# Kernel tuning notes

Measured on AMD Instinct MI355X. Metric: run time of the kernel, lower is better.

## Reference

```python
import jax, jax.numpy as jnp
import numpy as np

B, N, M = 8, 1024, 1024
D_MODEL, D_HEAD, M_BITS = 1024, 128, 32
SCALE = 1.0 / np.sqrt(M_BITS)


def setup_inputs() -> dict:
    key = jax.random.key(0)
    ks = jax.random.split(key, 11)
    w_std = 1.0 / np.sqrt(D_MODEL)  # ~ nn.Linear init scale
    f32 = jnp.float32
    return {
        "Q": jax.random.normal(ks[0], (B, N, D_MODEL), dtype=f32),
        "K": jax.random.normal(ks[1], (B, M, D_MODEL), dtype=f32),
        "V": jax.random.normal(ks[2], (B, M, D_MODEL), dtype=f32),
        "Wq_boolean": jax.random.normal(ks[3], (D_MODEL, M_BITS), dtype=f32) * w_std,
        "Wk_boolean": jax.random.normal(ks[4], (D_MODEL, M_BITS), dtype=f32) * w_std,
        "Wq_tropical": jax.random.normal(ks[5], (D_MODEL, M_BITS), dtype=f32) * w_std,
        "Wk_tropical": jax.random.normal(ks[6], (D_MODEL, M_BITS), dtype=f32) * w_std,
        "Wq_real": jax.random.normal(ks[7], (D_MODEL, M_BITS), dtype=f32) * w_std,
        "Wk_real": jax.random.normal(ks[8], (D_MODEL, M_BITS), dtype=f32) * w_std,
        "Wv": jax.random.normal(ks[9], (D_MODEL, D_HEAD), dtype=f32) * w_std,
        "fusion_weights": jnp.ones((3,), dtype=f32),
        "mask": jnp.ones((B, N, M), dtype=jnp.int32),
    }


def _tropical_sim(Qe, Ke):
    # max-plus (tropical) witness similarity: sim[b,n,m] = max_d (Qe[b,n,d] + Ke[b,m,d])
    # loop over the small fixed bit dim (M_BITS=32) to avoid a [B,N,M,M_BITS] tensor
    acc = Qe[:, :, 0][:, :, None] + Ke[:, :, 0][:, None, :]
    for b in range(1, M_BITS):
        acc = jnp.maximum(acc, Qe[:, :, b][:, :, None] + Ke[:, :, b][:, None, :])
    return acc  # [B,N,M]


def reference(Q, K, V, Wq_boolean, Wk_boolean, Wq_tropical, Wk_tropical,
              Wq_real, Wk_real, Wv, fusion_weights, mask):
    # --- boolean monoid: hard-binarized codes, bit-match count ---
    Qb = (Q @ Wq_boolean > 0).astype(Q.dtype)   # [B,N,m]
    Kb = (K @ Wk_boolean > 0).astype(K.dtype)   # [B,M,m]
    sim_bool = (jnp.einsum('bnd,bmd->bnm', Qb, Kb)
                + jnp.einsum('bnd,bmd->bnm', 1.0 - Qb, 1.0 - Kb))
    # --- tropical monoid: max-plus over continuous codes ---
    sim_trop = _tropical_sim(Q @ Wq_tropical, K @ Wk_tropical)
    # --- real monoid: inner product of continuous codes ---
    sim_real = jnp.einsum('bnd,bmd->bnm', Q @ Wq_real, K @ Wk_real)
    # --- learned fusion + scaled softmax attention ---
    w = jax.nn.softmax(fusion_weights)
    scores = (w[0] * sim_bool + w[1] * sim_trop + w[2] * sim_real) * SCALE
    scores = jnp.where(mask == 0, -jnp.inf, scores)
    attn = jax.nn.softmax(scores, axis=-1)     # [B,N,M]  (dropout: eval mode, identity)
    out = jnp.einsum('bnm,bmh->bnh', attn, V @ Wv)  # [B,N,d_head]
    return out, attn
```

## Files before the change

kernel.cpp:

```cpp
#include <hip/hip_runtime.h>
#include <stdint.h>
#include <math.h>


#define SCALE_F 0.17677669529663687f

typedef float4 f4;

__device__ __forceinline__ float f4c(const f4 v, int i) {
    return i == 0 ? v.x : (i == 1 ? v.y : (i == 2 ? v.z : v.w));
}


__global__ __launch_bounds__(256)
void proj_qk_kernel(const float* __restrict__ Q, const float* __restrict__ K,
                    const float* __restrict__ Wqb, const float* __restrict__ Wkb,
                    const float* __restrict__ Wqt, const float* __restrict__ Wkt,
                    const float* __restrict__ Wqr, const float* __restrict__ Wkr,
                    float* __restrict__ Pq, float* __restrict__ Pk) {
    const int t = threadIdx.x;
    const int bx = blockIdx.x;
    const int by = blockIdx.y;
    const int side = blockIdx.z;
    const float* __restrict__ X  = side ? K   : Q;
    const float* __restrict__ Wb = side ? Wkb : Wqb;
    const float* __restrict__ Wt = side ? Wkt : Wqt;
    const float* __restrict__ Wr = side ? Wkr : Wqr;
    float* __restrict__ P = side ? Pk : Pq;

    __shared__ float Xs[128][68];
    __shared__ float Ws[64][96];

    const int r0 = bx * 128;
    const int rt = t >> 3;
    const int cg = t & 7;

    float acc[4][12];
    #pragma unroll
    for (int i = 0; i < 4; ++i)
        #pragma unroll
        for (int j = 0; j < 12; ++j) acc[i][j] = 0.f;

    for (int dc = 0; dc < 4; ++dc) {
        const int dbase = by * 256 + dc * 64;
        #pragma unroll
        for (int k2 = 0; k2 < 8; ++k2) {
            int idx = t + k2 * 256;
            int r = idx >> 4, c4 = idx & 15;
            *(f4*)&Xs[r][c4 * 4] = *(const f4*)&X[(size_t)(r0 + r) * 1024 + dbase + c4 * 4];
        }
        #pragma unroll
        for (int k2 = 0; k2 < 6; ++k2) {
            int idx = t + k2 * 256;
            int d = idx / 24, c4 = idx % 24;
            const float* __restrict__ src = (c4 < 8) ? Wb : ((c4 < 16) ? Wt : Wr);
            *(f4*)&Ws[d][c4 * 4] = *(const f4*)&src[(size_t)(dbase + d) * 32 + (c4 & 7) * 4];
        }
        __syncthreads();
        for (int dd = 0; dd < 64; dd += 4) {
            f4 xf[4];
            #pragma unroll
            for (int i = 0; i < 4; ++i) xf[i] = *(const f4*)&Xs[4 * rt + i][dd];
            #pragma unroll
            for (int d2 = 0; d2 < 4; ++d2) {
                f4 wf[3];
                #pragma unroll
                for (int jj = 0; jj < 3; ++jj)
                    wf[jj] = *(const f4*)&Ws[dd + d2][12 * cg + 4 * jj];
                #pragma unroll
                for (int i = 0; i < 4; ++i) {
                    const float xv = f4c(xf[i], d2);
                    #pragma unroll
                    for (int jj = 0; jj < 3; ++jj) {
                        acc[i][jj * 4 + 0] += xv * wf[jj].x;
                        acc[i][jj * 4 + 1] += xv * wf[jj].y;
                        acc[i][jj * 4 + 2] += xv * wf[jj].z;
                        acc[i][jj * 4 + 3] += xv * wf[jj].w;
                    }
                }
            }
        }
        __syncthreads();
    }
    #pragma unroll
    for (int i = 0; i < 4; ++i) {
        size_t base = ((size_t)by * 8192 + r0 + 4 * rt + i) * 96 + 12 * cg;
        *(f4*)&P[base + 0] = make_float4(acc[i][0], acc[i][1], acc[i][2],  acc[i][3]);
        *(f4*)&P[base + 4] = make_float4(acc[i][4], acc[i][5], acc[i][6],  acc[i][7]);
        *(f4*)&P[base + 8] = make_float4(acc[i][8], acc[i][9], acc[i][10], acc[i][11]);
    }
}

__global__ __launch_bounds__(256)
void proj_v_kernel(const float* __restrict__ V, const float* __restrict__ Wv,
                   float* __restrict__ P) {
    const int t = threadIdx.x;
    const int r0 = blockIdx.x * 128;
    const int by = blockIdx.y;
    __shared__ float Xs[128][36];
    __shared__ float Ws[32][128];
    const int rt = t >> 3, cg = t & 7;

    float acc[4][16];
    #pragma unroll
    for (int i = 0; i < 4; ++i)
        #pragma unroll
        for (int j = 0; j < 16; ++j) acc[i][j] = 0.f;

    for (int dc = 0; dc < 8; ++dc) {
        const int dbase = by * 256 + dc * 32;
        #pragma unroll
        for (int k2 = 0; k2 < 4; ++k2) {
            int idx = t + k2 * 256;
            int r = idx >> 3, c4 = idx & 7;
            *(f4*)&Xs[r][c4 * 4] = *(const f4*)&V[(size_t)(r0 + r) * 1024 + dbase + c4 * 4];
        }
        #pragma unroll
        for (int k2 = 0; k2 < 4; ++k2) {
            int idx = t + k2 * 256;
            int d = idx >> 5, c4 = idx & 31;
            *(f4*)&Ws[d][c4 * 4] = *(const f4*)&Wv[(size_t)(dbase + d) * 128 + c4 * 4];
        }
        __syncthreads();
        for (int dd = 0; dd < 32; dd += 4) {
            f4 xf[4];
            #pragma unroll
            for (int i = 0; i < 4; ++i) xf[i] = *(const f4*)&Xs[4 * rt + i][dd];
            #pragma unroll
            for (int d2 = 0; d2 < 4; ++d2) {
                f4 wf[4];
                #pragma unroll
                for (int jj = 0; jj < 4; ++jj)
                    wf[jj] = *(const f4*)&Ws[dd + d2][16 * cg + 4 * jj];
                #pragma unroll
                for (int i = 0; i < 4; ++i) {
                    const float xv = f4c(xf[i], d2);
                    #pragma unroll
                    for (int jj = 0; jj < 4; ++jj) {
                        acc[i][jj * 4 + 0] += xv * wf[jj].x;
                        acc[i][jj * 4 + 1] += xv * wf[jj].y;
                        acc[i][jj * 4 + 2] += xv * wf[jj].z;
                        acc[i][jj * 4 + 3] += xv * wf[jj].w;
                    }
                }
            }
        }
        __syncthreads();
    }
    #pragma unroll
    for (int i = 0; i < 4; ++i) {
        size_t base = ((size_t)by * 8192 + r0 + 4 * rt + i) * 128 + 16 * cg;
        #pragma unroll
        for (int jj = 0; jj < 4; ++jj)
            *(f4*)&P[base + 4 * jj] = make_float4(acc[i][jj * 4 + 0], acc[i][jj * 4 + 1],
                                                  acc[i][jj * 4 + 2], acc[i][jj * 4 + 3]);
    }
}


__global__ __launch_bounds__(256)
void pack_codes_kernel(const float* __restrict__ Pq, const float* __restrict__ Pk,
                       float* __restrict__ Qt, float* __restrict__ Qr,
                       float* __restrict__ Kt, float* __restrict__ Kr) {
    const int gid = blockIdx.x * 256 + threadIdx.x;
    const int side = blockIdx.y;
    const float* __restrict__ P = side ? Pk : Pq;
    const int row = gid >> 6, c = gid & 63;
    float s = 0.f;
    #pragma unroll
    for (int g = 0; g < 4; ++g) s += P[((size_t)g * 8192 + row) * 96 + 32 + c];
    float* __restrict__ dT = side ? Kt : Qt;
    float* __restrict__ dR = side ? Kr : Qr;
    if (c < 32) dT[row * 32 + c] = s;
    else        dR[row * 32 + (c - 32)] = s;
}

__global__ __launch_bounds__(256)
void pack_bits_kernel(const float* __restrict__ Pq, const float* __restrict__ Pk,
                      uint32_t* __restrict__ Qbits, uint32_t* __restrict__ Kbits) {
    const int gid = blockIdx.x * 256 + threadIdx.x;
    const int side = blockIdx.y;
    const float* __restrict__ P = side ? Pk : Pq;
    const int row = gid >> 5, c = gid & 31;
    float s = 0.f;
    #pragma unroll
    for (int g = 0; g < 4; ++g) s += P[((size_t)g * 8192 + row) * 96 + c];
    const unsigned long long bm = __ballot(s > 0.f);
    uint32_t* __restrict__ bits = side ? Kbits : Qbits;
    const int lane = threadIdx.x & 63;
    if (lane == 0)       bits[row] = (uint32_t)bm;
    else if (lane == 32) bits[row] = (uint32_t)(bm >> 32);
}

__global__ __launch_bounds__(256)
void reduce4_kernel(const float* __restrict__ P, float* __restrict__ dst) {
    const int gid = blockIdx.x * 256 + threadIdx.x;
    f4 a = ((const f4*)P)[gid];
    f4 b = ((const f4*)P)[262144 + gid];
    f4 c = ((const f4*)P)[2 * 262144 + gid];
    f4 d = ((const f4*)P)[3 * 262144 + gid];
    ((f4*)dst)[gid] = make_float4(a.x + b.x + c.x + d.x, a.y + b.y + c.y + d.y,
                                  a.z + b.z + c.z + d.z, a.w + b.w + c.w + d.w);
}


__global__ __launch_bounds__(256)
void scores_kernel(const float* __restrict__ Qt, const float* __restrict__ Qr,
                   const float* __restrict__ Kt, const float* __restrict__ Kr,
                   const uint32_t* __restrict__ Qbits, const uint32_t* __restrict__ Kbits,
                   const float* __restrict__ fw, float* __restrict__ attn) {
    const int t = threadIdx.x;
    const int m0 = blockIdx.x * 64;
    const int n0 = blockIdx.y * 64;
    const int b  = blockIdx.z;

    __shared__ float Qt_s[64][36], Qr_s[64][36];
    __shared__ float KtT[32][68],  KrT[32][68];
    __shared__ uint32_t qb_s[64], kb_s[64];

    #pragma unroll
    for (int k2 = 0; k2 < 2; ++k2) {
        int idx = t + k2 * 256;
        int r = idx >> 3, c4 = idx & 7;
        *(f4*)&Qt_s[r][c4 * 4] = *(const f4*)&Qt[(size_t)(b * 1024 + n0 + r) * 32 + c4 * 4];
        *(f4*)&Qr_s[r][c4 * 4] = *(const f4*)&Qr[(size_t)(b * 1024 + n0 + r) * 32 + c4 * 4];
        f4 vt = *(const f4*)&Kt[(size_t)(b * 1024 + m0 + r) * 32 + c4 * 4];
        f4 vr = *(const f4*)&Kr[(size_t)(b * 1024 + m0 + r) * 32 + c4 * 4];
        KtT[c4 * 4 + 0][r] = vt.x; KtT[c4 * 4 + 1][r] = vt.y;
        KtT[c4 * 4 + 2][r] = vt.z; KtT[c4 * 4 + 3][r] = vt.w;
        KrT[c4 * 4 + 0][r] = vr.x; KrT[c4 * 4 + 1][r] = vr.y;
        KrT[c4 * 4 + 2][r] = vr.z; KrT[c4 * 4 + 3][r] = vr.w;
    }
    if (t < 64)       qb_s[t] = Qbits[b * 1024 + n0 + t];
    else if (t < 128) kb_s[t - 64] = Kbits[b * 1024 + m0 + (t - 64)];
    __syncthreads();

    const float f0 = fw[0], f1 = fw[1], f2 = fw[2];
    const float fm = fmaxf(f0, fmaxf(f1, f2));
    const float e0 = __expf(f0 - fm), e1 = __expf(f1 - fm), e2 = __expf(f2 - fm);
    const float wi = 1.f / (e0 + e1 + e2);
    const float w0 = e0 * wi, w1 = e1 * wi, w2 = e2 * wi;

    const int rg = t >> 4, mg = t & 15;

    float tacc[4][4], racc[4][4];
    #pragma unroll
    for (int i = 0; i < 4; ++i)
        #pragma unroll
        for (int j = 0; j < 4; ++j) { tacc[i][j] = -INFINITY; racc[i][j] = 0.f; }

    for (int d0 = 0; d0 < 32; d0 += 4) {
        f4 qt4[4], qr4[4];
        #pragma unroll
        for (int i = 0; i < 4; ++i) {
            qt4[i] = *(const f4*)&Qt_s[4 * rg + i][d0];
            qr4[i] = *(const f4*)&Qr_s[4 * rg + i][d0];
        }
        #pragma unroll
        for (int d2 = 0; d2 < 4; ++d2) {
            const f4 kt = *(const f4*)&KtT[d0 + d2][4 * mg];
            const f4 kr = *(const f4*)&KrT[d0 + d2][4 * mg];
            #pragma unroll
            for (int i = 0; i < 4; ++i) {
                const float qtv = f4c(qt4[i], d2);
                const float qrv = f4c(qr4[i], d2);
                tacc[i][0] = fmaxf(tacc[i][0], qtv + kt.x);
                tacc[i][1] = fmaxf(tacc[i][1], qtv + kt.y);
                tacc[i][2] = fmaxf(tacc[i][2], qtv + kt.z);
                tacc[i][3] = fmaxf(tacc[i][3], qtv + kt.w);
                racc[i][0] += qrv * kr.x;
                racc[i][1] += qrv * kr.y;
                racc[i][2] += qrv * kr.z;
                racc[i][3] += qrv * kr.w;
            }
        }
    }

    uint32_t qb[4], kb[4];
    #pragma unroll
    for (int i = 0; i < 4; ++i) { qb[i] = qb_s[4 * rg + i]; kb[i] = kb_s[4 * mg + i]; }
    #pragma unroll
    for (int i = 0; i < 4; ++i) {
        float sj[4];
        #pragma unroll
        for (int j = 0; j < 4; ++j) {
            const float cnt = (float)(32 - __popc(qb[i] ^ kb[j]));
            sj[j] = (w0 * cnt + w1 * tacc[i][j] + w2 * racc[i][j]) * SCALE_F;
        }
        *(f4*)&attn[(size_t)(b * 1024 + n0 + 4 * rg + i) * 1024 + m0 + 4 * mg] =
            make_float4(sj[0], sj[1], sj[2], sj[3]);
    }
}


__global__ __launch_bounds__(256)
void softmax_kernel(float* __restrict__ attn, const int* __restrict__ mask) {
    const int row = blockIdx.x;
    const int t = threadIdx.x;
    const f4  s4 = ((const f4*)attn)[(size_t)row * 256 + t];
    const int4 m4 = ((const int4*)mask)[(size_t)row * 256 + t];
    const float v0 = m4.x ? s4.x : -INFINITY;
    const float v1 = m4.y ? s4.y : -INFINITY;
    const float v2 = m4.z ? s4.z : -INFINITY;
    const float v3 = m4.w ? s4.w : -INFINITY;

    float tm = fmaxf(fmaxf(v0, v1), fmaxf(v2, v3));
    #pragma unroll
    for (int off = 32; off >= 1; off >>= 1) tm = fmaxf(tm, __shfl_xor(tm, off, 64));
    __shared__ float rmax[4], rsum[4];
    if ((t & 63) == 0) rmax[t >> 6] = tm;
    __syncthreads();
    const float gm = fmaxf(fmaxf(rmax[0], rmax[1]), fmaxf(rmax[2], rmax[3]));

    const float x0 = m4.x ? __expf(v0 - gm) : 0.f;
    const float x1 = m4.y ? __expf(v1 - gm) : 0.f;
    const float x2 = m4.z ? __expf(v2 - gm) : 0.f;
    const float x3 = m4.w ? __expf(v3 - gm) : 0.f;
    float ts = (x0 + x1) + (x2 + x3);
    #pragma unroll
    for (int off = 32; off >= 1; off >>= 1) ts += __shfl_xor(ts, off, 64);
    if ((t & 63) == 0) rsum[t >> 6] = ts;
    __syncthreads();
    const float inv = 1.f / (((rsum[0] + rsum[1]) + (rsum[2] + rsum[3])));

    ((f4*)attn)[(size_t)row * 256 + t] = make_float4(x0 * inv, x1 * inv, x2 * inv, x3 * inv);
}


__global__ __launch_bounds__(256)
void pv_kernel(const float* __restrict__ attn, const float* __restrict__ Vp,
               float* __restrict__ Pout) {
    const int t = threadIdx.x;
    const int row0 = blockIdx.x * 64;
    const int ms = blockIdx.y;
    const int b = row0 >> 10;
    __shared__ float As[64][68];
    __shared__ float Vs[64][128];
    const int rt = t >> 4, hg = t & 15;

    float acc[4][8];
    #pragma unroll
    for (int i = 0; i < 4; ++i)
        #pragma unroll
        for (int j = 0; j < 8; ++j) acc[i][j] = 0.f;

    for (int mc = 0; mc < 4; ++mc) {
        const int mb = ms * 256 + mc * 64;
        #pragma unroll
        for (int k2 = 0; k2 < 4; ++k2) {
            int idx = t + k2 * 256;
            int r = idx >> 4, c4 = idx & 15;
            *(f4*)&As[r][c4 * 4] = *(const f4*)&attn[(size_t)(row0 + r) * 1024 + mb + c4 * 4];
        }
        #pragma unroll
        for (int k2 = 0; k2 < 8; ++k2) {
            int idx = t + k2 * 256;
            int m = idx >> 5, c4 = idx & 31;
            *(f4*)&Vs[m][c4 * 4] = *(const f4*)&Vp[(size_t)(b * 1024 + mb + m) * 128 + c4 * 4];
        }
        __syncthreads();
        for (int m = 0; m < 64; ++m) {
            const f4 u0 = *(const f4*)&Vs[m][hg * 8];
            const f4 u1 = *(const f4*)&Vs[m][hg * 8 + 4];
            #pragma unroll
            for (int i = 0; i < 4; ++i) {
                const float a = As[4 * rt + i][m];
                acc[i][0] += a * u0.x; acc[i][1] += a * u0.y;
                acc[i][2] += a * u0.z; acc[i][3] += a * u0.w;
                acc[i][4] += a * u1.x; acc[i][5] += a * u1.y;
                acc[i][6] += a * u1.z; acc[i][7] += a * u1.w;
            }
        }
        __syncthreads();
    }
    #pragma unroll
    for (int i = 0; i < 4; ++i) {
        size_t base = ((size_t)ms * 8192 + row0 + 4 * rt + i) * 128 + hg * 8;
        *(f4*)&Pout[base]     = make_float4(acc[i][0], acc[i][1], acc[i][2], acc[i][3]);
        *(f4*)&Pout[base + 4] = make_float4(acc[i][4], acc[i][5], acc[i][6], acc[i][7]);
    }
}


extern "C" void kernel_launch(void* const* d_in, const int* in_sizes, int n_in,
                              void* d_out, int out_size, void* d_ws, size_t ws_size,
                              hipStream_t stream) {
    const float* Q   = (const float*)d_in[0];
    const float* K   = (const float*)d_in[1];
    const float* V   = (const float*)d_in[2];
    const float* Wqb = (const float*)d_in[3];
    const float* Wkb = (const float*)d_in[4];
    const float* Wqt = (const float*)d_in[5];
    const float* Wkt = (const float*)d_in[6];
    const float* Wqr = (const float*)d_in[7];
    const float* Wkr = (const float*)d_in[8];
    const float* Wv  = (const float*)d_in[9];
    const float* fw  = (const float*)d_in[10];
    const int*  mask = (const int*)d_in[11];

    float* ws = (float*)d_ws;
    float* Qt = ws;
    float* Qr = Qt + 262144;
    float* Kt = Qr + 262144;
    float* Kr = Kt + 262144;
    float* Vp = Kr + 262144;
    uint32_t* Qbits = (uint32_t*)(Vp + 1048576);
    uint32_t* Kbits = Qbits + 8192;
    float* Pbig = (float*)(Kbits + 8192);

    float* out  = (float*)d_out;
    float* attn = out + 1048576;
    float* Pq = attn;
    float* Pk = attn + 3145728;

    proj_qk_kernel<<<dim3(64, 4, 2), 256, 0, stream>>>(Q, K, Wqb, Wkb, Wqt, Wkt, Wqr, Wkr, Pq, Pk);
    proj_v_kernel<<<dim3(64, 4), 256, 0, stream>>>(V, Wv, Pbig);
    pack_codes_kernel<<<dim3(2048, 2), 256, 0, stream>>>(Pq, Pk, Qt, Qr, Kt, Kr);
    pack_bits_kernel<<<dim3(1024, 2), 256, 0, stream>>>(Pq, Pk, Qbits, Kbits);
    reduce4_kernel<<<1024, 256, 0, stream>>>(Pbig, Vp);
    scores_kernel<<<dim3(16, 16, 8), 256, 0, stream>>>(Qt, Qr, Kt, Kr, Qbits, Kbits, fw, attn);
    softmax_kernel<<<8192, 256, 0, stream>>>(attn, mask);
    pv_kernel<<<dim3(128, 4), 256, 0, stream>>>(attn, Vp, Pbig);
    reduce4_kernel<<<1024, 256, 0, stream>>>(Pbig, out);
}
```

Measured before the change: 313.7 us.

## Move projections and PV onto bf16 MFMA with split-precision emulation of fp32

Replaces the fp32 FMA projection GEMMs (Q/K codes, V) and the attention-times-V GEMM with MFMA bf16 kernels that split each fp32 operand into two or three bf16 parts to keep fp32-like accuracy. The boolean codes get three-term splitting so that sign decisions stay stable. The projection kernel now fuses the split-K reduction, code packing and bit ballots directly, which removes the pack_codes, pack_bits and reduce4 kernels and their intermediate buffers. It also adds a weight-conversion kernel and uses double-buffered swizzled LDS tiles. The risk is small numerical differences from the bf16 split, which could flip boolean bits near zero.

Result: faster. 284.8 us (-9.2%).

```diff
diff --git a/kernel.cpp b/kernel.cpp
--- a/kernel.cpp
+++ b/kernel.cpp
@@ -6,208 +6,399 @@
 #define SCALE_F 0.17677669529663687f
 
 typedef float4 f4;
-
+typedef __attribute__((ext_vector_type(8))) short s16x8;
+typedef __attribute__((ext_vector_type(8))) unsigned short u16x8;
+typedef __attribute__((ext_vector_type(4))) float f32x4;
+
+__device__ __forceinline__ unsigned short f2bf(float x) {
+    unsigned u = __float_as_uint(x);
+    return (unsigned short)((u + 0x7FFFu + ((u >> 16) & 1u)) >> 16);
+}
+__device__ __forceinline__ float bf2f(unsigned short h) {
+    return __uint_as_float(((unsigned)h) << 16);
+}
 __device__ __forceinline__ float f4c(const f4 v, int i) {
     return i == 0 ? v.x : (i == 1 ? v.y : (i == 2 ? v.z : v.w));
 }
 
+#define MFMA16(a, b, c) __builtin_amdgcn_mfma_f32_16x16x32_bf16((a), (b), (c), 0, 0, 0)
+
+
+__global__ __launch_bounds__(256)
+void conv_w_kernel(const float* __restrict__ Wqb, const float* __restrict__ Wkb,
+                   const float* __restrict__ Wqt, const float* __restrict__ Wkt,
+                   const float* __restrict__ Wqr, const float* __restrict__ Wkr,
+                   const float* __restrict__ Wv,
+                   unsigned short* __restrict__ Wh, unsigned short* __restrict__ Wm,
+                   unsigned short* __restrict__ Wl3,
+                   unsigned short* __restrict__ Wvh, unsigned short* __restrict__ Wvm) {
+    __shared__ float T[256][33];
+    const int t = threadIdx.x;
+    const int bid = blockIdx.x;
+    const float* src;
+    int kb, outRowBase, srcStride, srcColBase, side = 0;
+    bool isQK, isBool;
+    if (bid < 24) {
+        side = bid / 12;
+        int cb = (bid % 12) / 4;
+        kb = bid & 3;
+        const float* mats[6] = {Wqb, Wqt, Wqr, Wkb, Wkt, Wkr};
+        src = mats[side * 3 + cb];
+        srcStride = 32; srcColBase = 0;
+        outRowBase = side * 96 + cb * 32;
+        isQK = true; isBool = (cb == 0);
+    } else {
+        int v = bid - 24;
+        int hb = v >> 2; kb = v & 3;
+        src = Wv; srcStride = 128; srcColBase = hb * 32;
+        outRowBase = hb * 32;
+        isQK = false; isBool = false;
+    }
+    #pragma unroll
+    for (int i = 0; i < 8; ++i) {
+        int idx = t + i * 256;
+        int r = idx >> 3, c4 = idx & 7;
+        f4 v = *(const f4*)&src[(size_t)(kb * 256 + r) * srcStride + srcColBase + c4 * 4];
+        T[r][c4 * 4 + 0] = v.x; T[r][c4 * 4 + 1] = v.y;
+        T[r][c4 * 4 + 2] = v.z; T[r][c4 * 4 + 3] = v.w;
+    }
+    __syncthreads();
+    const int col = t >> 3, kseg = t & 7;
+    unsigned short* dh = isQK ? Wh : Wvh;
+    unsigned short* dm = isQK ? Wm : Wvm;
+    size_t obase = (size_t)(outRowBase + col) * 1024 + kb * 256 + kseg * 32;
+    u16x8 ph[4], pm[4], pl[4];
+    #pragma unroll
+    for (int i = 0; i < 32; ++i) {
+        float x = T[kseg * 32 + i][col];
+        unsigned short hb_ = f2bf(x);
+        float r1 = x - bf2f(hb_);
+        unsigned short mb_ = f2bf(r1);
+        float r2 = r1 - bf2f(mb_);
+        ph[i >> 3][i & 7] = hb_;
+        pm[i >> 3][i & 7] = mb_;
+        pl[i >> 3][i & 7] = f2bf(r2);
+    }
+    #pragma unroll
+    for (int i = 0; i < 4; ++i) {
+        *(u16x8*)&dh[obase + i * 8] = ph[i];
+        *(u16x8*)&dm[obase + i * 8] = pm[i];
+    }
+    if (isBool) {
+        size_t lbase = (size_t)(side * 32 + col) * 1024 + kb * 256 + kseg * 32;
+        #pragma unroll
+        for (int i = 0; i < 4; ++i) *(u16x8*)&Wl3[lbase + i * 8] = pl[i];
+    }
+}
+
 
 __global__ __launch_bounds__(256)
 void proj_qk_kernel(const float* __restrict__ Q, const float* __restrict__ K,
-                    const float* __restrict__ Wqb, const float* __restrict__ Wkb,
-                    const float* __restrict__ Wqt, const float* __restrict__ Wkt,
-                    const float* __restrict__ Wqr, const float* __restrict__ Wkr,
-                    float* __restrict__ Pq, float* __restrict__ Pk) {
-    const int t = threadIdx.x;
-    const int bx = blockIdx.x;
-    const int by = blockIdx.y;
-    const int side = blockIdx.z;
-    const float* __restrict__ X  = side ? K   : Q;
-    const float* __restrict__ Wb = side ? Wkb : Wqb;
-    const float* __restrict__ Wt = side ? Wkt : Wqt;
-    const float* __restrict__ Wr = side ? Wkr : Wqr;
-    float* __restrict__ P = side ? Pk : Pq;
-
-    __shared__ float Xs[128][68];
-    __shared__ float Ws[64][96];
-
-    const int r0 = bx * 128;
-    const int rt = t >> 3;
-    const int cg = t & 7;
-
-    float acc[4][12];
-    #pragma unroll
-    for (int i = 0; i < 4; ++i)
-        #pragma unroll
-        for (int j = 0; j < 12; ++j) acc[i][j] = 0.f;
-
-    for (int dc = 0; dc < 4; ++dc) {
-        const int dbase = by * 256 + dc * 64;
-        #pragma unroll
-        for (int k2 = 0; k2 < 8; ++k2) {
-            int idx = t + k2 * 256;
-            int r = idx >> 4, c4 = idx & 15;
-            *(f4*)&Xs[r][c4 * 4] = *(const f4*)&X[(size_t)(r0 + r) * 1024 + dbase + c4 * 4];
-        }
-        #pragma unroll
-        for (int k2 = 0; k2 < 6; ++k2) {
-            int idx = t + k2 * 256;
-            int d = idx / 24, c4 = idx % 24;
-            const float* __restrict__ src = (c4 < 8) ? Wb : ((c4 < 16) ? Wt : Wr);
-            *(f4*)&Ws[d][c4 * 4] = *(const f4*)&src[(size_t)(dbase + d) * 32 + (c4 & 7) * 4];
+                    const unsigned short* __restrict__ Wh, const unsigned short* __restrict__ Wm,
+                    const unsigned short* __restrict__ Wl3,
+                    float* __restrict__ Qt, float* __restrict__ Qr,
+                    float* __restrict__ Kt, float* __restrict__ Kr,
+                    unsigned* __restrict__ Qbits, unsigned* __restrict__ Kbits) {
+    const int t = threadIdx.x, lane = t & 63, w = t >> 6;
+    const int side = blockIdx.y;
+    const int gr0 = blockIdx.x * 32;
+    const float* __restrict__ X = side ? K : Q;
+    float* __restrict__ Tt = side ? Kt : Qt;
+    float* __restrict__ Tr = side ? Kr : Qr;
+    unsigned* __restrict__ Tb = side ? Kbits : Qbits;
+
+    __shared__ unsigned short Ah[2][1024], Am[2][1024], Al[2][1024];
+    __shared__ unsigned short BhS[2][3072], BmS[2][3072], BlS[2][1024];
+    __shared__ unsigned sb[32];
+    if (t < 32) sb[t] = 0;
+
+    const int arow = t >> 2, asp = t & 3;
+    const bool adoA = t < 128;
+    const size_t aXbase = (size_t)(gr0 + arow) * 1024 + (asp ^ (arow & 3)) * 8;
+    const int aLds = arow * 32 + asp * 8;
+
+    int blvl[4]; size_t bsrc[4]; int blds[4]; bool bok[4];
+    #pragma unroll
+    for (int i = 0; i < 4; ++i) {
+        int s = t + i * 256;
+        bok[i] = s < 896;
+        int lvl = (s < 384) ? 0 : (s < 768 ? 1 : 2);
+        int cs = s - (lvl == 0 ? 0 : (lvl == 1 ? 384 : 768));
+        int col = cs >> 2, sp = cs & 3;
+        blvl[i] = lvl;
+        int colRow = (lvl == 2) ? (side * 32 + col) : (side * 96 + col);
+        bsrc[i] = (size_t)colRow * 1024 + (sp ^ (col & 3)) * 8;
+        blds[i] = col * 32 + sp * 8;
+    }
+
+    const int wr0 = (w >= 2) ? 16 : 0;
+    const bool isBoolWave = ((w & 1) == 0);
+    const int kg = lane >> 4;
+    const int frow = wr0 + (lane & 15);
+    const int aoff = frow * 32 + (kg ^ (frow & 3)) * 8;
+
+    f32x4 acc[4];
+    #pragma unroll
+    for (int i = 0; i < 4; ++i) acc[i] = f32x4{0.f, 0.f, 0.f, 0.f};
+
+    if (adoA) {
+        f4 v0 = *(const f4*)&X[aXbase + 0];
+        f4 v1 = *(const f4*)&X[aXbase + 4];
+        u16x8 h, m, l;
+        #pragma unroll
+        for (int j = 0; j < 8; ++j) {
+            float x = (j < 4) ? f4c(v0, j) : f4c(v1, j - 4);
+            unsigned short hb_ = f2bf(x);
+            float r1 = x - bf2f(hb_);
+            unsigned short mb_ = f2bf(r1);
+            float r2 = r1 - bf2f(mb_);
+            h[j] = hb_; m[j] = mb_; l[j] = f2bf(r2);
+        }
+        *(u16x8*)&Ah[0][aLds] = h; *(u16x8*)&Am[0][aLds] = m; *(u16x8*)&Al[0][aLds] = l;
+    }
+    #pragma unroll
+    for (int i = 0; i < 4; ++i) if (bok[i]) {
+        const unsigned short* sp_ = (blvl[i] == 0) ? Wh : (blvl[i] == 1 ? Wm : Wl3);
+        u16x8 v = *(const u16x8*)&sp_[bsrc[i]];
+        if (blvl[i] == 0)      *(u16x8*)&BhS[0][blds[i]] = v;
+        else if (blvl[i] == 1) *(u16x8*)&BmS[0][blds[i]] = v;
+        else                   *(u16x8*)&BlS[0][blds[i]] = v;
+    }
+    __syncthreads();
+
+    for (int kc = 0; kc < 32; ++kc) {
+        const int cur = kc & 1, nxt = cur ^ 1;
+        const bool more = (kc + 1) < 32;
+        f4 av0, av1;
+        u16x8 bv[4];
+        if (more) {
+            const size_t ko = (size_t)(kc + 1) * 32;
+            if (adoA) {
+                av0 = *(const f4*)&X[aXbase + ko];
+                av1 = *(const f4*)&X[aXbase + ko + 4];
+            }
+            #pragma unroll
+            for (int i = 0; i < 4; ++i) if (bok[i]) {
+                const unsigned short* sp_ = (blvl[i] == 0) ? Wh : (blvl[i] == 1 ? Wm : Wl3);
+                bv[i] = *(const u16x8*)&sp_[bsrc[i] + ko];
+            }
+        }
+        s16x8 a1 = *(const s16x8*)&Ah[cur][aoff];
+        s16x8 a2 = *(const s16x8*)&Am[cur][aoff];
+        if (isBoolWave) {
+            s16x8 a3 = *(const s16x8*)&Al[cur][aoff];
+            #pragma unroll
+            for (int cf = 0; cf < 2; ++cf) {
+                int col = 16 * cf + (lane & 15);
+                int boff = col * 32 + (kg ^ (col & 3)) * 8;
+                s16x8 b1 = *(const s16x8*)&BhS[cur][boff];
+                s16x8 b2 = *(const s16x8*)&BmS[cur][boff];
+                s16x8 b3 = *(const s16x8*)&BlS[cur][boff];
+                acc[cf] = MFMA16(a1, b1, acc[cf]);
+                acc[cf] = MFMA16(a1, b2, acc[cf]);
+                acc[cf] = MFMA16(a2, b1, acc[cf]);
+                acc[cf] = MFMA16(a2, b2, acc[cf]);
+                acc[cf] = MFMA16(a1, b3, acc[cf]);
+                acc[cf] = MFMA16(a3, b1, acc[cf]);
+            }
+        } else {
+            #pragma unroll
+            for (int cf = 0; cf < 4; ++cf) {
+                int col = 32 + 16 * cf + (lane & 15);
+                int boff = col * 32 + (kg ^ (col & 3)) * 8;
+                s16x8 b1 = *(const s16x8*)&BhS[cur][boff];
+                s16x8 b2 = *(const s16x8*)&BmS[cur][boff];
+                acc[cf] = MFMA16(a1, b1, acc[cf]);
+                acc[cf] = MFMA16(a1, b2, acc[cf]);
+                acc[cf] = MFMA16(a2, b1, acc[cf]);
+            }
+        }
+        if (more) {
+            if (adoA) {
+                u16x8 h, m, l;
+                #pragma unroll
+                for (int j = 0; j < 8; ++j) {
+                    float x = (j < 4) ? f4c(av0, j) : f4c(av1, j - 4);
+                    unsigned short hb_ = f2bf(x);
+                    float r1 = x - bf2f(hb_);
+                    unsigned short mb_ = f2bf(r1);
+                    float r2 = r1 - bf2f(mb_);
+                    h[j] = hb_; m[j] = mb_; l[j] = f2bf(r2);
+                }
+                *(u16x8*)&Ah[nxt][aLds] = h; *(u16x8*)&Am[nxt][aLds] = m; *(u16x8*)&Al[nxt][aLds] = l;
+            }
+            #pragma unroll
+            for (int i = 0; i < 4; ++i) if (bok[i]) {
+                if (blvl[i] == 0)      *(u16x8*)&BhS[nxt][blds[i]] = bv[i];
+                else if (blvl[i] == 1) *(u16x8*)&BmS[nxt][blds[i]] = bv[i];
+                else                   *(u16x8*)&BlS[nxt][blds[i]] = bv[i];
+            }
         }
         __syncthreads();
-        for (int dd = 0; dd < 64; dd += 4) {
-            f4 xf[4];
-            #pragma unroll
-            for (int i = 0; i < 4; ++i) xf[i] = *(const f4*)&Xs[4 * rt + i][dd];
-            #pragma unroll
-            for (int d2 = 0; d2 < 4; ++d2) {
-                f4 wf[3];
+    }
+
+    if (isBoolWave) {
+        #pragma unroll
+        for (int cf = 0; cf < 2; ++cf)
+            #pragma unroll
+            for (int r = 0; r < 4; ++r) {
+                unsigned long long bm = __ballot(acc[cf][r] > 0.f);
+                if (lane == 0) {
+                    #pragma unroll
+                    for (int g = 0; g < 4; ++g)
+                        sb[wr0 + g * 4 + r] |=
+                            (unsigned)((bm >> (16 * g)) & 0xFFFFull) << (16 * cf);
+                }
+            }
+    } else {
+        #pragma unroll
+        for (int cf = 0; cf < 4; ++cf)
+            #pragma unroll
+            for (int r = 0; r < 4; ++r) {
+                int rowg = gr0 + wr0 + kg * 4 + r;
+                int c = 16 * (cf & 1) + (lane & 15);
+                if (cf < 2) Tt[(size_t)rowg * 32 + c] = acc[cf][r];
+                else        Tr[(size_t)rowg * 32 + c] = acc[cf][r];
+            }
+    }
+    __syncthreads();
+    if (t < 32) Tb[gr0 + t] = sb[t];
+}
+
+
+__global__ __launch_bounds__(256)
+void proj_v_kernel(const float* __restrict__ V,
+                   const unsigned short* __restrict__ Wvh, const unsigned short* __restrict__ Wvm,
+                   unsigned short* __restrict__ VpTh, unsigned short* __restrict__ VpTl) {
+    const int t = threadIdx.x, lane = t & 63, w = t >> 6;
+    const int gr0 = blockIdx.x * 32;
+    const int b = gr0 >> 10, m_in_b = gr0 & 1023;
+
+    __shared__ unsigned short Ah[2][1024], Am[2][1024];
+    __shared__ unsigned short BhS[2][4096], BmS[2][4096];
+    __shared__ float T[32][132];
+
+    const int arow = t >> 2, asp = t & 3;
+    const bool adoA = t < 128;
+    const size_t aXbase = (size_t)(gr0 + arow) * 1024 + (asp ^ (arow & 3)) * 8;
+    const int aLds = arow * 32 + asp * 8;
+
+    int blvl[4]; size_t bsrc[4]; int blds[4];
+    #pragma unroll
+    for (int i = 0; i < 4; ++i) {
+        int s = t + i * 256;
+        blvl[i] = s >> 9;
+        int cs = s & 511;
+        int col = cs >> 2, sp = cs & 3;
+        bsrc[i] = (size_t)col * 1024 + (sp ^ (col & 3)) * 8;
+        blds[i] = col * 32 + sp * 8;
+    }
+
+    const int wr0 = (w >= 2) ? 16 : 0;
+    const int hbase = (w & 1) ? 64 : 0;
+    const int kg = lane >> 4;
+    const int frow = wr0 + (lane & 15);
+    const int aoff = frow * 32 + (kg ^ (frow & 3)) * 8;
+
+    f32x4 acc[4];
+    #pragma unroll
+    for (int i = 0; i < 4; ++i) acc[i] = f32x4{0.f, 0.f, 0.f, 0.f};
+
+    if (adoA) {
+        f4 v0 = *(const f4*)&V[aXbase + 0];
+        f4 v1 = *(const f4*)&V[aXbase + 4];
+        u16x8 h, m;
+        #pragma unroll
+        for (int j = 0; j < 8; ++j) {
+            float x = (j < 4) ? f4c(v0, j) : f4c(v1, j - 4);
+            unsigned short hb_ = f2bf(x);
+            h[j] = hb_; m[j] = f2bf(x - bf2f(hb_));
+        }
+        *(u16x8*)&Ah[0][aLds] = h; *(u16x8*)&Am[0][aLds] = m;
+    }
+    #pragma unroll
+    for (int i = 0; i < 4; ++i) {
+        const unsigned short* sp_ = blvl[i] ? Wvm : Wvh;
+        u16x8 v = *(const u16x8*)&sp_[bsrc[i]];
+        if (blvl[i]) *(u16x8*)&BmS[0][blds[i]] = v;
+        else         *(u16x8*)&BhS[0][blds[i]] = v;
+    }
+    __syncthreads();
+
+    for (int kc = 0; kc < 32; ++kc) {
+        const int cur = kc & 1, nxt = cur ^ 1;
+        const bool more = (kc + 1) < 32;
+        f4 av0, av1;
+        u16x8 bv[4];
+        if (more) {
+            const size_t ko = (size_t)(kc + 1) * 32;
+            if (adoA) {
+                av0 = *(const f4*)&V[aXbase + ko];
+                av1 = *(const f4*)&V[aXbase + ko + 4];
+            }
+            #pragma unroll
+            for (int i = 0; i < 4; ++i) {
+                const unsigned short* sp_ = blvl[i] ? Wvm : Wvh;
+                bv[i] = *(const u16x8*)&sp_[bsrc[i] + ko];
+            }
+        }
+        s16x8 a1 = *(const s16x8*)&Ah[cur][aoff];
+        s16x8 a2 = *(const s16x8*)&Am[cur][aoff];
+        #pragma unroll
+        for (int cf = 0; cf < 4; ++cf) {
+            int col = hbase + 16 * cf + (lane & 15);
+            int boff = col * 32 + (kg ^ (col & 3)) * 8;
+            s16x8 b1 = *(const s16x8*)&BhS[cur][boff];
+            s16x8 b2 = *(const s16x8*)&BmS[cur][boff];
+            acc[cf] = MFMA16(a1, b1, acc[cf]);
+            acc[cf] = MFMA16(a1, b2, acc[cf]);
+            acc[cf] = MFMA16(a2, b1, acc[cf]);
+        }
+        if (more) {
+            if (adoA) {
+                u16x8 h, m;
                 #pragma unroll
-                for (int jj = 0; jj < 3; ++jj)
-                    wf[jj] = *(const f4*)&Ws[dd + d2][12 * cg + 4 * jj];
-                #pragma unroll
-                for (int i = 0; i < 4; ++i) {
-                    const float xv = f4c(xf[i], d2);
-                    #pragma unroll
-                    for (int jj = 0; jj < 3; ++jj) {
-                        acc[i][jj * 4 + 0] += xv * wf[jj].x;
-                        acc[i][jj * 4 + 1] += xv * wf[jj].y;
-                        acc[i][jj * 4 + 2] += xv * wf[jj].z;
-                        acc[i][jj * 4 + 3] += xv * wf[jj].w;
-                    }
+                for (int j = 0; j < 8; ++j) {
+                    float x = (j < 4) ? f4c(av0, j) : f4c(av1, j - 4);
+                    unsigned short hb_ = f2bf(x);
+                    h[j] = hb_; m[j] = f2bf(x - bf2f(hb_));
                 }
+                *(u16x8*)&Ah[nxt][aLds] = h; *(u16x8*)&Am[nxt][aLds] = m;
+            }
+            #pragma unroll
+            for (int i = 0; i < 4; ++i) {
+                if (blvl[i]) *(u16x8*)&BmS[nxt][blds[i]] = bv[i];
+                else         *(u16x8*)&BhS[nxt][blds[i]] = bv[i];
             }
         }
         __syncthreads();
     }
-    #pragma unroll
-    for (int i = 0; i < 4; ++i) {
-        size_t base = ((size_t)by * 8192 + r0 + 4 * rt + i) * 96 + 12 * cg;
-        *(f4*)&P[base + 0] = make_float4(acc[i][0], acc[i][1], acc[i][2],  acc[i][3]);
-        *(f4*)&P[base + 4] = make_float4(acc[i][4], acc[i][5], acc[i][6],  acc[i][7]);
-        *(f4*)&P[base + 8] = make_float4(acc[i][8], acc[i][9], acc[i][10], acc[i][11]);
-    }
-}
-
-__global__ __launch_bounds__(256)
-void proj_v_kernel(const float* __restrict__ V, const float* __restrict__ Wv,
-                   float* __restrict__ P) {
-    const int t = threadIdx.x;
-    const int r0 = blockIdx.x * 128;
-    const int by = blockIdx.y;
-    __shared__ float Xs[128][36];
-    __shared__ float Ws[32][128];
-    const int rt = t >> 3, cg = t & 7;
-
-    float acc[4][16];
-    #pragma unroll
-    for (int i = 0; i < 4; ++i)
-        #pragma unroll
-        for (int j = 0; j < 16; ++j) acc[i][j] = 0.f;
-
-    for (int dc = 0; dc < 8; ++dc) {
-        const int dbase = by * 256 + dc * 32;
-        #pragma unroll
-        for (int k2 = 0; k2 < 4; ++k2) {
-            int idx = t + k2 * 256;
-            int r = idx >> 3, c4 = idx & 7;
-            *(f4*)&Xs[r][c4 * 4] = *(const f4*)&V[(size_t)(r0 + r) * 1024 + dbase + c4 * 4];
-        }
-        #pragma unroll
-        for (int k2 = 0; k2 < 4; ++k2) {
-            int idx = t + k2 * 256;
-            int d = idx >> 5, c4 = idx & 31;
-            *(f4*)&Ws[d][c4 * 4] = *(const f4*)&Wv[(size_t)(dbase + d) * 128 + c4 * 4];
-        }
-        __syncthreads();
-        for (int dd = 0; dd < 32; dd += 4) {
-            f4 xf[4];
-            #pragma unroll
-            for (int i = 0; i < 4; ++i) xf[i] = *(const f4*)&Xs[4 * rt + i][dd];
-            #pragma unroll
-            for (int d2 = 0; d2 < 4; ++d2) {
-                f4 wf[4];
-                #pragma unroll
-                for (int jj = 0; jj < 4; ++jj)
-                    wf[jj] = *(const f4*)&Ws[dd + d2][16 * cg + 4 * jj];
-                #pragma unroll
-                for (int i = 0; i < 4; ++i) {
-                    const float xv = f4c(xf[i], d2);
-                    #pragma unroll
-                    for (int jj = 0; jj < 4; ++jj) {
-                        acc[i][jj * 4 + 0] += xv * wf[jj].x;
-                        acc[i][jj * 4 + 1] += xv * wf[jj].y;
-                        acc[i][jj * 4 + 2] += xv * wf[jj].z;
-                        acc[i][jj * 4 + 3] += xv * wf[jj].w;
-                    }
-                }
-            }
-        }
-        __syncthreads();
-    }
-    #pragma unroll
-    for (int i = 0; i < 4; ++i) {
-        size_t base = ((size_t)by * 8192 + r0 + 4 * rt + i) * 128 + 16 * cg;
-        #pragma unroll
-        for (int jj = 0; jj < 4; ++jj)
-            *(f4*)&P[base + 4 * jj] = make_float4(acc[i][jj * 4 + 0], acc[i][jj * 4 + 1],
-                                                  acc[i][jj * 4 + 2], acc[i][jj * 4 + 3]);
-    }
-}
-
-
-__global__ __launch_bounds__(256)
-void pack_codes_kernel(const float* __restrict__ Pq, const float* __restrict__ Pk,
-                       float* __restrict__ Qt, float* __restrict__ Qr,
-                       float* __restrict__ Kt, float* __restrict__ Kr) {
-    const int gid = blockIdx.x * 256 + threadIdx.x;
-    const int side = blockIdx.y;
-    const float* __restrict__ P = side ? Pk : Pq;
-    const int row = gid >> 6, c = gid & 63;
-    float s = 0.f;
-    #pragma unroll
-    for (int g = 0; g < 4; ++g) s += P[((size_t)g * 8192 + row) * 96 + 32 + c];
-    float* __restrict__ dT = side ? Kt : Qt;
-    float* __restrict__ dR = side ? Kr : Qr;
-    if (c < 32) dT[row * 32 + c] = s;
-    else        dR[row * 32 + (c - 32)] = s;
-}
-
-__global__ __launch_bounds__(256)
-void pack_bits_kernel(const float* __restrict__ Pq, const float* __restrict__ Pk,
-                      uint32_t* __restrict__ Qbits, uint32_t* __restrict__ Kbits) {
-    const int gid = blockIdx.x * 256 + threadIdx.x;
-    const int side = blockIdx.y;
-    const float* __restrict__ P = side ? Pk : Pq;
-    const int row = gid >> 5, c = gid & 31;
-    float s = 0.f;
-    #pragma unroll
-    for (int g = 0; g < 4; ++g) s += P[((size_t)g * 8192 + row) * 96 + c];
-    const unsigned long long bm = __ballot(s > 0.f);
-    uint32_t* __restrict__ bits = side ? Kbits : Qbits;
-    const int lane = threadIdx.x & 63;
-    if (lane == 0)       bits[row] = (uint32_t)bm;
-    else if (lane == 32) bits[row] = (uint32_t)(bm >> 32);
-}
-
-__global__ __launch_bounds__(256)
-void reduce4_kernel(const float* __restrict__ P, float* __restrict__ dst) {
-    const int gid = blockIdx.x * 256 + threadIdx.x;
-    f4 a = ((const f4*)P)[gid];
-    f4 b = ((const f4*)P)[262144 + gid];
-    f4 c = ((const f4*)P)[2 * 262144 + gid];
-    f4 d = ((const f4*)P)[3 * 262144 + gid];
-    ((f4*)dst)[gid] = make_float4(a.x + b.x + c.x + d.x, a.y + b.y + c.y + d.y,
-                                  a.z + b.z + c.z + d.z, a.w + b.w + c.w + d.w);
+
+    #pragma unroll
+    for (int cf = 0; cf < 4; ++cf)
+        #pragma unroll
+        for (int r = 0; r < 4; ++r)
+            T[wr0 + kg * 4 + r][hbase + 16 * cf + (lane & 15)] = acc[cf][r];
+    __syncthreads();
+    const int h = t >> 1, m0 = (t & 1) * 16;
+    u16x8 hh[2], ll[2];
+    #pragma unroll
+    for (int i = 0; i < 16; ++i) {
+        float x = T[m0 + i][h];
+        unsigned short hb_ = f2bf(x);
+        hh[i >> 3][i & 7] = hb_;
+        ll[i >> 3][i & 7] = f2bf(x - bf2f(hb_));
+    }
+    size_t obase = (size_t)(b * 128 + h) * 1024 + m_in_b + m0;
+    *(u16x8*)&VpTh[obase] = hh[0]; *(u16x8*)&VpTh[obase + 8] = hh[1];
+    *(u16x8*)&VpTl[obase] = ll[0]; *(u16x8*)&VpTl[obase + 8] = ll[1];
 }
 
 
 __global__ __launch_bounds__(256)
 void scores_kernel(const float* __restrict__ Qt, const float* __restrict__ Qr,
                    const float* __restrict__ Kt, const float* __restrict__ Kr,
-                   const uint32_t* __restrict__ Qbits, const uint32_t* __restrict__ Kbits,
+                   const unsigned* __restrict__ Qbits, const unsigned* __restrict__ Kbits,
                    const float* __restrict__ fw, float* __restrict__ attn) {
     const int t = threadIdx.x;
     const int m0 = blockIdx.x * 64;
@@ -216,7 +407,7 @@
 
     __shared__ float Qt_s[64][36], Qr_s[64][36];
     __shared__ float KtT[32][68],  KrT[32][68];
-    __shared__ uint32_t qb_s[64], kb_s[64];
+    __shared__ unsigned qb_s[64], kb_s[64];
 
     #pragma unroll
     for (int k2 = 0; k2 < 2; ++k2) {
@@ -276,7 +467,7 @@
         }
     }
 
-    uint32_t qb[4], kb[4];
+    unsigned qb[4], kb[4];
     #pragma unroll
     for (int i = 0; i < 4; ++i) { qb[i] = qb_s[4 * rg + i]; kb[i] = kb_s[4 * mg + i]; }
     #pragma unroll
@@ -328,57 +519,118 @@
 
 
 __global__ __launch_bounds__(256)
-void pv_kernel(const float* __restrict__ attn, const float* __restrict__ Vp,
-               float* __restrict__ Pout) {
-    const int t = threadIdx.x;
-    const int row0 = blockIdx.x * 64;
-    const int ms = blockIdx.y;
-    const int b = row0 >> 10;
-    __shared__ float As[64][68];
-    __shared__ float Vs[64][128];
-    const int rt = t >> 4, hg = t & 15;
-
-    float acc[4][8];
-    #pragma unroll
-    for (int i = 0; i < 4; ++i)
-        #pragma unroll
-        for (int j = 0; j < 8; ++j) acc[i][j] = 0.f;
-
-    for (int mc = 0; mc < 4; ++mc) {
-        const int mb = ms * 256 + mc * 64;
-        #pragma unroll
-        for (int k2 = 0; k2 < 4; ++k2) {
-            int idx = t + k2 * 256;
-            int r = idx >> 4, c4 = idx & 15;
-            *(f4*)&As[r][c4 * 4] = *(const f4*)&attn[(size_t)(row0 + r) * 1024 + mb + c4 * 4];
-        }
-        #pragma unroll
-        for (int k2 = 0; k2 < 8; ++k2) {
-            int idx = t + k2 * 256;
-            int m = idx >> 5, c4 = idx & 31;
-            *(f4*)&Vs[m][c4 * 4] = *(const f4*)&Vp[(size_t)(b * 1024 + mb + m) * 128 + c4 * 4];
+void pv_kernel(const float* __restrict__ attn,
+               const unsigned short* __restrict__ VpTh, const unsigned short* __restrict__ VpTl,
+               float* __restrict__ out) {
+    const int t = threadIdx.x, lane = t & 63, w = t >> 6;
+    const int gr0 = blockIdx.x * 32;
+    const int b = gr0 >> 10;
+
+    __shared__ unsigned short Ah[2][1024], Am[2][1024];
+    __shared__ unsigned short BhS[2][4096], BmS[2][4096];
+
+    const int arow = t >> 2, asp = t & 3;
+    const bool adoA = t < 128;
+    const size_t aXbase = (size_t)(gr0 + arow) * 1024 + (asp ^ (arow & 3)) * 8;
+    const int aLds = arow * 32 + asp * 8;
+
+    int blvl[4]; size_t bsrc[4]; int blds[4];
+    #pragma unroll
+    for (int i = 0; i < 4; ++i) {
+        int s = t + i * 256;
+        blvl[i] = s >> 9;
+        int cs = s & 511;
+        int col = cs >> 2, sp = cs & 3;
+        bsrc[i] = (size_t)(b * 128 + col) * 1024 + (sp ^ (col & 3)) * 8;
+        blds[i] = col * 32 + sp * 8;
+    }
+
+    const int wr0 = (w >= 2) ? 16 : 0;
+    const int hbase = (w & 1) ? 64 : 0;
+    const int kg = lane >> 4;
+    const int frow = wr0 + (lane & 15);
+    const int aoff = frow * 32 + (kg ^ (frow & 3)) * 8;
+
+    f32x4 acc[4];
+    #pragma unroll
+    for (int i = 0; i < 4; ++i) acc[i] = f32x4{0.f, 0.f, 0.f, 0.f};
+
+    if (adoA) {
+        f4 v0 = *(const f4*)&attn[aXbase + 0];
+        f4 v1 = *(const f4*)&attn[aXbase + 4];
+        u16x8 h, m;
+        #pragma unroll
+        for (int j = 0; j < 8; ++j) {
+            float x = (j < 4) ? f4c(v0, j) : f4c(v1, j - 4);
+            unsigned short hb_ = f2bf(x);
+            h[j] = hb_; m[j] = f2bf(x - bf2f(hb_));
+        }
+        *(u16x8*)&Ah[0][aLds] = h; *(u16x8*)&Am[0][aLds] = m;
+    }
+    #pragma unroll
+    for (int i = 0; i < 4; ++i) {
+        const unsigned short* sp_ = blvl[i] ? VpTl : VpTh;
+        u16x8 v = *(const u16x8*)&sp_[bsrc[i]];
+        if (blvl[i]) *(u16x8*)&BmS[0][blds[i]] = v;
+        else         *(u16x8*)&BhS[0][blds[i]] = v;
+    }
+    __syncthreads();
+
+    for (int kc = 0; kc < 32; ++kc) {
+        const int cur = kc & 1, nxt = cur ^ 1;
+        const bool more = (kc + 1) < 32;
+        f4 av0, av1;
+        u16x8 bv[4];
+        if (more) {
+            const size_t ko = (size_t)(kc + 1) * 32;
+            if (adoA) {
+                av0 = *(const f4*)&attn[aXbase + ko];
+                av1 = *(const f4*)&attn[aXbase + ko + 4];
+            }
+            #pragma unroll
+            for (int i = 0; i < 4; ++i) {
+                const unsigned short* sp_ = blvl[i] ? VpTl : VpTh;
+                bv[i] = *(const u16x8*)&sp_[bsrc[i] + ko];
+            }
+        }
+        s16x8 a1 = *(const s16x8*)&Ah[cur][aoff];
+        s16x8 a2 = *(const s16x8*)&Am[cur][aoff];
+        #pragma unroll
+        for (int cf = 0; cf < 4; ++cf) {
+            int col = hbase + 16 * cf + (lane & 15);
+            int boff = col * 32 + (kg ^ (col & 3)) * 8;
+            s16x8 b1 = *(const s16x8*)&BhS[cur][boff];
+            s16x8 b2 = *(const s16x8*)&BmS[cur][boff];
+            acc[cf] = MFMA16(a1, b1, acc[cf]);
+            acc[cf] = MFMA16(a1, b2, acc[cf]);
+            acc[cf] = MFMA16(a2, b1, acc[cf]);
+        }
+        if (more) {
+            if (adoA) {
+                u16x8 h, m;
+                #pragma unroll
+                for (int j = 0; j < 8; ++j) {
+                    float x = (j < 4) ? f4c(av0, j) : f4c(av1, j - 4);
+                    unsigned short hb_ = f2bf(x);
+                    h[j] = hb_; m[j] = f2bf(x - bf2f(hb_));
+                }
+                *(u16x8*)&Ah[nxt][aLds] = h; *(u16x8*)&Am[nxt][aLds] = m;
+            }
+            #pragma unroll
+            for (int i = 0; i < 4; ++i) {
+                if (blvl[i]) *(u16x8*)&BmS[nxt][blds[i]] = bv[i];
+                else         *(u16x8*)&BhS[nxt][blds[i]] = bv[i];
+            }
         }
         __syncthreads();
-        for (int m = 0; m < 64; ++m) {
-            const f4 u0 = *(const f4*)&Vs[m][hg * 8];
-            const f4 u1 = *(const f4*)&Vs[m][hg * 8 + 4];
-            #pragma unroll
-            for (int i = 0; i < 4; ++i) {
-                const float a = As[4 * rt + i][m];
-                acc[i][0] += a * u0.x; acc[i][1] += a * u0.y;
-                acc[i][2] += a * u0.z; acc[i][3] += a * u0.w;
-                acc[i][4] += a * u1.x; acc[i][5] += a * u1.y;
-                acc[i][6] += a * u1.z; acc[i][7] += a * u1.w;
-            }
-        }
-        __syncthreads();
-    }
-    #pragma unroll
-    for (int i = 0; i < 4; ++i) {
-        size_t base = ((size_t)ms * 8192 + row0 + 4 * rt + i) * 128 + hg * 8;
-        *(f4*)&Pout[base]     = make_float4(acc[i][0], acc[i][1], acc[i][2], acc[i][3]);
-        *(f4*)&Pout[base + 4] = make_float4(acc[i][4], acc[i][5], acc[i][6], acc[i][7]);
-    }
+    }
+
+    #pragma unroll
+    for (int cf = 0; cf < 4; ++cf)
+        #pragma unroll
+        for (int r = 0; r < 4; ++r)
+            out[(size_t)(gr0 + wr0 + kg * 4 + r) * 128 + hbase + 16 * cf + (lane & 15)] =
+                acc[cf][r];
 }
 
 
@@ -399,27 +651,30 @@
     const int*  mask = (const int*)d_in[11];
 
     float* ws = (float*)d_ws;
-    float* Qt = ws;
-    float* Qr = Qt + 262144;
-    float* Kt = Qr + 262144;
-    float* Kr = Kt + 262144;
-    float* Vp = Kr + 262144;
-    uint32_t* Qbits = (uint32_t*)(Vp + 1048576);
-    uint32_t* Kbits = Qbits + 8192;
-    float* Pbig = (float*)(Kbits + 8192);
+    float* QtW = ws;
+    float* QrW = QtW + 262144;
+    float* KtW = QrW + 262144;
+    float* KrW = KtW + 262144;
+    unsigned* QbitsW = (unsigned*)(KrW + 262144);
+    unsigned* KbitsW = QbitsW + 8192;
+    unsigned short* Wh   = (unsigned short*)(KbitsW + 8192);
+    unsigned short* Wm   = Wh + 196608;
+    unsigned short* Wl3  = Wm + 196608;
+    unsigned short* Wvh  = Wl3 + 65536;
+    unsigned short* Wvm  = Wvh + 131072;
+    unsigned short* VpTh = Wvm + 131072;
+    unsigned short* VpTl = VpTh + 1048576;
 
     float* out  = (float*)d_out;
     float* attn = out + 1048576;
-    float* Pq = attn;
-    float* Pk = attn + 3145728;
-
-    proj_qk_kernel<<<dim3(64, 4, 2), 256, 0, stream>>>(Q, K, Wqb, Wkb, Wqt, Wkt, Wqr, Wkr, Pq, Pk);
-    proj_v_kernel<<<dim3(64, 4), 256, 0, stream>>>(V, Wv, Pbig);
-    pack_codes_kernel<<<dim3(2048, 2), 256, 0, stream>>>(Pq, Pk, Qt, Qr, Kt, Kr);
-    pack_bits_kernel<<<dim3(1024, 2), 256, 0, stream>>>(Pq, Pk, Qbits, Kbits);
-    reduce4_kernel<<<1024, 256, 0, stream>>>(Pbig, Vp);
-    scores_kernel<<<dim3(16, 16, 8), 256, 0, stream>>>(Qt, Qr, Kt, Kr, Qbits, Kbits, fw, attn);
+
+    conv_w_kernel<<<40, 256, 0, stream>>>(Wqb, Wkb, Wqt, Wkt, Wqr, Wkr, Wv,
+                                          Wh, Wm, Wl3, Wvh, Wvm);
+    proj_qk_kernel<<<dim3(256, 2), 256, 0, stream>>>(Q, K, Wh, Wm, Wl3,
+                                                     QtW, QrW, KtW, KrW, QbitsW, KbitsW);
+    proj_v_kernel<<<256, 256, 0, stream>>>(V, Wvh, Wvm, VpTh, VpTl);
+    scores_kernel<<<dim3(16, 16, 8), 256, 0, stream>>>(QtW, QrW, KtW, KrW,
+                                                       QbitsW, KbitsW, fw, attn);
     softmax_kernel<<<8192, 256, 0, stream>>>(attn, mask);
-    pv_kernel<<<dim3(128, 4), 256, 0, stream>>>(attn, Vp, Pbig);
-    reduce4_kernel<<<1024, 256, 0, stream>>>(Pbig, out);
-}
+    pv_kernel<<<256, 256, 0, stream>>>(attn, VpTh, VpTl, out);
+}
```
